# Optimization experiments

Hardware: AMD Instinct MI355X
Metric: run time of the kernel (lower is better)

The kernel has to match this reference:

```python
import jax, jax.numpy as jnp
import numpy as np

B, S, DIM_IN, DIM_K, DIM_V = 4, 2048, 512, 2048, 64


def setup_inputs() -> dict:
    key = jax.random.key(0)
    k1, k2, k3, k4 = jax.random.split(key, 4)
    x = jax.random.normal(k1, (B, S, DIM_IN), dtype=jnp.float32)
    # nn.Linear(dim_in, d, bias=False) -> stored transposed here so y = x @ W
    Wq = jax.random.normal(k2, (DIM_IN, DIM_K), dtype=jnp.float32) / np.sqrt(DIM_IN)
    Wk = jax.random.normal(k3, (DIM_IN, DIM_K), dtype=jnp.float32) / np.sqrt(DIM_IN)
    Wv = jax.random.normal(k4, (DIM_IN, DIM_V), dtype=jnp.float32) / np.sqrt(DIM_IN)
    return {"x": x, "Wq": Wq, "Wk": Wk, "Wv": Wv}


def reference(x, Wq, Wk, Wv):
    dim_k = Wq.shape[-1]
    q = x @ Wq            # [B, S, dim_k]
    k = x @ Wk            # [B, S, dim_k]
    v = x @ Wv            # [B, S, dim_v]
    scores = jnp.einsum("bqd,bkd->bqk", q, k)  # [B, S, S]
    # causal mask: disallow attending to strictly-future positions
    seq = scores.shape[-1]
    mask = jnp.triu(jnp.ones((seq, seq), dtype=bool), k=1)
    scores = jnp.where(mask[None, :, :], -jnp.inf, scores)
    attn = jax.nn.softmax(scores / np.sqrt(dim_k).astype(np.float32), axis=-1)
    return attn @ v       # [B, S, dim_v]
```

## Files before the change

kernel.cpp:

```cpp
#include <hip/hip_runtime.h>
#include <hip/hip_bf16.h>
#include <math.h>

using bf16 = __hip_bfloat16;
typedef __bf16 bf16x8 __attribute__((ext_vector_type(8)));
typedef float floatx4 __attribute__((ext_vector_type(4)));

constexpr int BB = 4, SS = 2048, DIN = 512, DKK = 2048, DVV = 64;
constexpr int ROWS = BB * SS;
constexpr int LDY = 640;

constexpr size_t XB_OFF  = 0;
constexpr size_t WQB_OFF = XB_OFF  + 8388608;
constexpr size_t WKB_OFF = WQB_OFF + 2097152;
constexpr size_t WT2_OFF = WKB_OFF + 2097152;
constexpr size_t MTP_OFF = WT2_OFF + 655360;
constexpr size_t YV_OFF  = MTP_OFF + 8388608;
constexpr size_t VT_OFF  = YV_OFF  + 10485760;
constexpr size_t PRT_OFF = VT_OFF  + 1048576;
constexpr size_t STA_OFF = PRT_OFF + 16777216;

__device__ __forceinline__ void async_copy16(const bf16* g, const unsigned short* l) {
    __builtin_amdgcn_global_load_lds((const __attribute__((address_space(1))) void*)g,
                                     (__attribute__((address_space(3))) void*)l, 16, 0, 0);
}

__global__ __launch_bounds__(256) void prep(const float* __restrict__ x,
                                            const float* __restrict__ Wq,
                                            const float* __restrict__ Wk,
                                            const float* __restrict__ Wv,
                                            bf16* __restrict__ xb,
                                            bf16* __restrict__ wqb,
                                            bf16* __restrict__ wkb,
                                            bf16* __restrict__ wt2) {
    __shared__ float tile[32][33];
    const int bid = blockIdx.x;
    const int tid = threadIdx.x;

    if (bid < 4096) {
        int i = bid * 256 + tid;
        float4 v = reinterpret_cast<const float4*>(x)[i];
        union { bf16 h[4]; ushort4 u; } cv;
        cv.h[0] = __float2bfloat16(v.x);
        cv.h[1] = __float2bfloat16(v.y);
        cv.h[2] = __float2bfloat16(v.z);
        cv.h[3] = __float2bfloat16(v.w);
        reinterpret_cast<ushort4*>(xb)[i] = cv.u;
    } else if (bid < 6144) {
        int i = (bid - 4096) * 256 + tid;
        const float* src = (i < 262144) ? Wq : Wk;
        bf16* dst = (i < 262144) ? wqb : wkb;
        int j = (i < 262144) ? i : i - 262144;
        float4 v = reinterpret_cast<const float4*>(src)[j];
        union { bf16 h[4]; ushort4 u; } cv;
        cv.h[0] = __float2bfloat16(v.x);
        cv.h[1] = __float2bfloat16(v.y);
        cv.h[2] = __float2bfloat16(v.z);
        cv.h[3] = __float2bfloat16(v.w);
        reinterpret_cast<ushort4*>(dst)[j] = cv.u;
    } else {
        int idx = bid - 6144;
        int n0 = (idx & 1) * 32;
        int k0 = (idx >> 1) * 32;
        int nn = tid & 31, kk8 = tid >> 5;
        #pragma unroll
        for (int p = 0; p < 4; ++p) {
            int k = p * 8 + kk8;
            tile[k][nn] = Wv[(long long)(k0 + k) * 64 + n0 + nn];
        }
        __syncthreads();
        int kk = tid & 31, nn8 = tid >> 5;
        #pragma unroll
        for (int p = 0; p < 4; ++p) {
            int n = p * 8 + nn8;
            wt2[(long long)(512 + n0 + n) * 512 + k0 + kk] = __float2bfloat16(tile[kk][n]);
        }
    }
}

__global__ __launch_bounds__(256) void gemm_mt(const bf16* __restrict__ A,
                                               const bf16* __restrict__ Bt,
                                               float* __restrict__ Cp) {
    __shared__ __align__(16) unsigned short As[128 * 64];
    __shared__ __align__(16) unsigned short Bs[128 * 64];

    const int tid = threadIdx.x;
    const int lane = tid & 63, wave = tid >> 6;

    const int wg = (blockIdx.x & 7) * 16 + (blockIdx.x >> 3);
    const int z = wg >> 4;
    const int tile = wg & 15;
    const long long m0 = (long long)(tile >> 2) * 128;
    const long long n0 = (long long)(tile & 3) * 128;
    const int koff = z * 256;

    const int rIn = lane >> 3;
    const int cSwz = ((lane & 7) ^ rIn) * 8;
    const int wm0 = (wave >> 1) * 64, wn0 = (wave & 1) * 64;
    const int l15 = lane & 15, quad = lane >> 4;
    const int sw7 = l15 & 7;

    floatx4 acc[4][4] = {};

    for (int k0 = koff; k0 < koff + 256; k0 += 64) {
        #pragma unroll
        for (int t0 = 0; t0 < 8; ++t0) {
            int t = t0 * 4 + wave;
            if (t < 16)
                async_copy16(A + (m0 + t * 8 + rIn) * 2048LL + k0 + cSwz, &As[t * 512]);
            else
                async_copy16(Bt + (n0 + (t - 16) * 8 + rIn) * 2048LL + k0 + cSwz, &Bs[(t - 16) * 512]);
        }
        __syncthreads();
        #pragma unroll
        for (int sk = 0; sk < 2; ++sk) {
            const int rchunk = (((sk << 2) | quad) ^ sw7) * 8;
            bf16x8 af[4], bfr[4];
            #pragma unroll
            for (int mi = 0; mi < 4; ++mi)
                af[mi] = *reinterpret_cast<const bf16x8*>(&As[(wm0 + mi * 16 + l15) * 64 + rchunk]);
            #pragma unroll
            for (int ni = 0; ni < 4; ++ni)
                bfr[ni] = *reinterpret_cast<const bf16x8*>(&Bs[(wn0 + ni * 16 + l15) * 64 + rchunk]);
            #pragma unroll
            for (int mi = 0; mi < 4; ++mi)
                #pragma unroll
                for (int ni = 0; ni < 4; ++ni)
                    acc[mi][ni] = __builtin_amdgcn_mfma_f32_16x16x32_bf16(af[mi], bfr[ni],
                                                                          acc[mi][ni], 0, 0, 0);
        }
        __syncthreads();
    }

    float* C = Cp + (long long)z * 262144;
    #pragma unroll
    for (int mi = 0; mi < 4; ++mi) {
        long long row0 = m0 + wm0 + mi * 16 + quad * 4;
        #pragma unroll
        for (int ni = 0; ni < 4; ++ni) {
            long long col = n0 + wn0 + ni * 16 + l15;
            #pragma unroll
            for (int r = 0; r < 4; ++r)
                C[(row0 + r) * 512 + col] = acc[mi][ni][r];
        }
    }
}

__global__ __launch_bounds__(256) void reduce_mt(const float4* __restrict__ part,
                                                 bf16* __restrict__ wt2) {
    int i = blockIdx.x * 256 + threadIdx.x;
    float4 s = {0.f, 0.f, 0.f, 0.f};
    #pragma unroll
    for (int t = 0; t < 8; ++t) {
        float4 a = part[(long long)t * 65536 + i];
        s.x += a.x; s.y += a.y; s.z += a.z; s.w += a.w;
    }
    union { bf16 h[4]; ushort4 u; } cv;
    cv.h[0] = __float2bfloat16(s.x);
    cv.h[1] = __float2bfloat16(s.y);
    cv.h[2] = __float2bfloat16(s.z);
    cv.h[3] = __float2bfloat16(s.w);
    reinterpret_cast<ushort4*>(wt2)[i] = cv.u;
}

__global__ __launch_bounds__(256) void gemm_proj(const bf16* __restrict__ A,
                                                 const bf16* __restrict__ Bt,
                                                 bf16* __restrict__ C,
                                                 bf16* __restrict__ vt) {
    __shared__ __align__(16) unsigned short As[128 * 64];
    __shared__ __align__(16) unsigned short Bs[128 * 64];

    const int tid = threadIdx.x;
    const int lane = tid & 63, wave = tid >> 6;

    const int wg = (blockIdx.x & 7) * 40 + (blockIdx.x >> 3);
    const long long m0 = (long long)(wg / 5) * 128;
    const long long n0 = (long long)(wg % 5) * 128;

    const int rIn = lane >> 3;
    const int cSwz = ((lane & 7) ^ rIn) * 8;
    const int wm0 = (wave >> 1) * 64, wn0 = (wave & 1) * 64;
    const int l15 = lane & 15, quad = lane >> 4;
    const int sw7 = l15 & 7;

    floatx4 acc[4][4] = {};

    for (int k0 = 0; k0 < DIN; k0 += 64) {
        #pragma unroll
        for (int t0 = 0; t0 < 8; ++t0) {
            int t = t0 * 4 + wave;
            if (t < 16)
                async_copy16(A + (m0 + t * 8 + rIn) * (long long)DIN + k0 + cSwz, &As[t * 512]);
            else
                async_copy16(Bt + (n0 + (t - 16) * 8 + rIn) * (long long)DIN + k0 + cSwz, &Bs[(t - 16) * 512]);
        }
        __syncthreads();
        #pragma unroll
        for (int sk = 0; sk < 2; ++sk) {
            const int rchunk = (((sk << 2) | quad) ^ sw7) * 8;
            bf16x8 af[4], bfr[4];
            #pragma unroll
            for (int mi = 0; mi < 4; ++mi)
                af[mi] = *reinterpret_cast<const bf16x8*>(&As[(wm0 + mi * 16 + l15) * 64 + rchunk]);
            #pragma unroll
            for (int ni = 0; ni < 4; ++ni)
                bfr[ni] = *reinterpret_cast<const bf16x8*>(&Bs[(wn0 + ni * 16 + l15) * 64 + rchunk]);
            #pragma unroll
            for (int mi = 0; mi < 4; ++mi)
                #pragma unroll
                for (int ni = 0; ni < 4; ++ni)
                    acc[mi][ni] = __builtin_amdgcn_mfma_f32_16x16x32_bf16(af[mi], bfr[ni],
                                                                          acc[mi][ni], 0, 0, 0);
        }
        __syncthreads();
    }

    if (n0 < 512) {
        #pragma unroll
        for (int mi = 0; mi < 4; ++mi) {
            long long row0 = m0 + wm0 + mi * 16 + quad * 4;
            #pragma unroll
            for (int ni = 0; ni < 4; ++ni) {
                long long col = n0 + wn0 + ni * 16 + l15;
                #pragma unroll
                for (int r = 0; r < 4; ++r)
                    C[(row0 + r) * (long long)LDY + col] = __float2bfloat16(acc[mi][ni][r]);
            }
        }
    } else if (!(wave & 1)) {
        const int b = (int)(m0 >> 11);
        const int sbase = ((int)m0 & 2047) + wm0;
        #pragma unroll
        for (int mi = 0; mi < 4; ++mi) {
            int s0 = sbase + mi * 16 + quad * 4;
            #pragma unroll
            for (int ni = 0; ni < 4; ++ni) {
                int j = ni * 16 + l15;
                union { bf16 h[4]; ushort4 u; } cv;
                #pragma unroll
                for (int r = 0; r < 4; ++r)
                    cv.h[r] = __float2bfloat16(acc[mi][ni][r]);
                *reinterpret_cast<ushort4*>(vt + ((long long)(b * DVV + j)) * SS + s0) = cv.u;
            }
        }
    }
}

__global__ __launch_bounds__(512) void attn_fused(const bf16* __restrict__ yv,
                                                  const bf16* __restrict__ xb,
                                                  const bf16* __restrict__ vt,
                                                  bf16* __restrict__ part,
                                                  float* __restrict__ stats) {
    constexpr int BK = 64;
    constexpr float SCALE = 0.022097086912079608f;

    __shared__ __align__(16) char smem[65536];
    unsigned short* As = (unsigned short*)smem;
    unsigned short* Bs = (unsigned short*)(smem + 32768);
    unsigned short* Ps = (unsigned short*)smem;
    unsigned short* Vs = (unsigned short*)(smem + 34816);
    float* smax = (float*)(smem + 52224);
    float* ssum = (float*)(smem + 53248);

    const int wg = (blockIdx.x & 7) * 17 + (blockIdx.x >> 3);
    int by = (int)((sqrtf(8.f * (float)wg + 1.f) - 1.f) * 0.5f);
    while ((by + 1) * (by + 2) / 2 <= wg) ++by;
    while (by * (by + 1) / 2 > wg) --by;
    const int bx = wg - by * (by + 1) / 2;
    const int b = blockIdx.z;

    const bf16* A  = yv + (long long)b * SS * LDY;
    const bf16* Bt = xb + (long long)b * SS * 512;

    const int tid = threadIdx.x;
    const int lane = tid & 63, wave = tid >> 6;
    const long long m0 = (long long)by * 128;
    const long long n0 = (long long)bx * 128;

    const int rIn = lane >> 3;
    const int cSwz = ((lane & 7) ^ rIn) * 8;
    const int wm0 = (wave >> 1) * 32, wn0 = (wave & 1) * 64;
    const int l15 = lane & 15, quad = lane >> 4;
    const int sw7 = l15 & 7;

    floatx4 acc[2][4] = {};

    uint4 vreg[2];
    #pragma unroll
    for (int p = 0; p < 2; ++p) {
        int j = (tid >> 4) + p * 32;
        int ch = tid & 15;
        vreg[p] = *reinterpret_cast<const uint4*>(
            vt + ((long long)b * DVV + j) * SS + n0 + ch * 8);
    }

    auto issue = [&](int buf, int k0) {
        #pragma unroll
        for (int t0 = 0; t0 < 4; ++t0) {
            int t = t0 * 8 + wave;
            if (t < 16)
                async_copy16(A + (m0 + t * 8 + rIn) * (long long)LDY + k0 + cSwz,
                             &As[buf * 8192 + t * 512]);
            else
                async_copy16(Bt + (n0 + (t - 16) * 8 + rIn) * 512LL + k0 + cSwz,
                             &Bs[buf * 8192 + (t - 16) * 512]);
        }
    };

    issue(0, 0);
    __syncthreads();
    for (int it = 0; it < DIN / BK; ++it) {
        const int cur = it & 1;
        if (it + 1 < DIN / BK) issue(cur ^ 1, (it + 1) * BK);
        #pragma unroll
        for (int sk = 0; sk < 2; ++sk) {
            const int rchunk = ((sk << 2) | quad) ^ sw7;
            bf16x8 af[2], bfr[4];
            #pragma unroll
            for (int mi = 0; mi < 2; ++mi)
                af[mi] = *reinterpret_cast<const bf16x8*>(
                    &As[cur * 8192 + (wm0 + mi * 16 + l15) * BK + rchunk * 8]);
            #pragma unroll
            for (int ni = 0; ni < 4; ++ni)
                bfr[ni] = *reinterpret_cast<const bf16x8*>(
                    &Bs[cur * 8192 + (wn0 + ni * 16 + l15) * BK + rchunk * 8]);
            #pragma unroll
            for (int mi = 0; mi < 2; ++mi)
                #pragma unroll
                for (int ni = 0; ni < 4; ++ni)
                    acc[mi][ni] = __builtin_amdgcn_mfma_f32_16x16x32_bf16(af[mi], bfr[ni],
                                                                          acc[mi][ni], 0, 0, 0);
        }
        __syncthreads();
    }

    #pragma unroll
    for (int mi = 0; mi < 2; ++mi)
        #pragma unroll
        for (int ni = 0; ni < 4; ++ni)
            #pragma unroll
            for (int r = 0; r < 4; ++r) {
                float v = acc[mi][ni][r] * SCALE;
                if (bx == by) {
                    int row = wm0 + mi * 16 + quad * 4 + r;
                    int col = wn0 + ni * 16 + l15;
                    if (col > row) v = -INFINITY;
                }
                acc[mi][ni][r] = v;
            }

    float rmax[2][4];
    #pragma unroll
    for (int mi = 0; mi < 2; ++mi)
        #pragma unroll
        for (int r = 0; r < 4; ++r) {
            float m = fmaxf(fmaxf(acc[mi][0][r], acc[mi][1][r]),
                            fmaxf(acc[mi][2][r], acc[mi][3][r]));
            #pragma unroll
            for (int msk = 8; msk >= 1; msk >>= 1) m = fmaxf(m, __shfl_xor(m, msk));
            rmax[mi][r] = m;
            if (l15 == 0) smax[(wm0 + mi * 16 + quad * 4 + r) * 2 + (wave & 1)] = m;
        }
    __syncthreads();
    #pragma unroll
    for (int mi = 0; mi < 2; ++mi)
        #pragma unroll
        for (int r = 0; r < 4; ++r) {
            int row = wm0 + mi * 16 + quad * 4 + r;
            rmax[mi][r] = fmaxf(smax[row * 2], smax[row * 2 + 1]);
        }

    #pragma unroll
    for (int mi = 0; mi < 2; ++mi)
        #pragma unroll
        for (int r = 0; r < 4; ++r) {
            float s = 0.f;
            #pragma unroll
            for (int ni = 0; ni < 4; ++ni) {
                float p = __expf(acc[mi][ni][r] - rmax[mi][r]);
                acc[mi][ni][r] = p;
                s += p;
            }
            #pragma unroll
            for (int msk = 8; msk >= 1; msk >>= 1) s += __shfl_xor(s, msk);
            if (l15 == 0) ssum[(wm0 + mi * 16 + quad * 4 + r) * 2 + (wave & 1)] = s;
        }
    #pragma unroll
    for (int mi = 0; mi < 2; ++mi) {
        int row = wm0 + mi * 16 + quad * 4;
        #pragma unroll
        for (int ni = 0; ni < 4; ++ni) {
            int col = wn0 + ni * 16 + l15;
            #pragma unroll
            for (int r = 0; r < 4; ++r)
                Ps[(row + r) * 136 + col] = (unsigned short)__bfloat16_as_ushort(__float2bfloat16(acc[mi][ni][r]));
        }
    }

    #pragma unroll
    for (int p = 0; p < 2; ++p) {
        int j = (tid >> 4) + p * 32;
        int ch = tid & 15;
        *reinterpret_cast<uint4*>(&Vs[j * 136 + ((ch ^ (j & 7)) * 8)]) = vreg[p];
    }
    __syncthreads();

    if (tid < 128) {
        float m = fmaxf(smax[tid * 2], smax[tid * 2 + 1]);
        float l = ssum[tid * 2] + ssum[tid * 2 + 1];
        long long o = (((long long)b * 16 + bx) * SS + m0 + tid) * 2;
        stats[o] = m;
        stats[o + 1] = l;
    }

    const int wmv = wave * 16;
    floatx4 accO[4] = {};
    #pragma unroll
    for (int sk = 0; sk < 4; ++sk) {
        bf16x8 af = *reinterpret_cast<const bf16x8*>(
            &Ps[(wmv + l15) * 136 + sk * 32 + quad * 8]);
        #pragma unroll
        for (int ni = 0; ni < 4; ++ni) {
            bf16x8 bfv = *reinterpret_cast<const bf16x8*>(
                &Vs[(ni * 16 + l15) * 136 + ((((sk << 2) | quad)) ^ sw7) * 8]);
            accO[ni] = __builtin_amdgcn_mfma_f32_16x16x32_bf16(af, bfv, accO[ni], 0, 0, 0);
        }
    }
    #pragma unroll
    for (int ni = 0; ni < 4; ++ni)
        #pragma unroll
        for (int r = 0; r < 4; ++r)
            part[(((long long)b * 16 + bx) * SS + m0 + wmv + quad * 4 + r) * 64 + ni * 16 + l15]
                = __float2bfloat16(accO[ni][r]);
}

__global__ __launch_bounds__(256) void combine(const bf16* __restrict__ part,
                                               const float* __restrict__ stats,
                                               float* __restrict__ out) {
    int tid = blockIdx.x * 256 + threadIdx.x;
    int row = tid >> 3;
    int col8 = (tid & 7) * 8;
    int b = row >> 11, s = row & (SS - 1);
    int nt = (s >> 7) + 1;

    float m[16], l[16], M = -INFINITY;
    #pragma unroll
    for (int t = 0; t < 16; ++t)
        if (t < nt) {
            long long o = (((long long)b * 16 + t) * SS + s) * 2;
            m[t] = stats[o];
            l[t] = stats[o + 1];
            M = fmaxf(M, m[t]);
        }
    float O[8] = {};
    float L = 0.f;
    #pragma unroll
    for (int t = 0; t < 16; ++t)
        if (t < nt) {
            float wgt = __expf(m[t] - M);
            L += wgt * l[t];
            union { uint4 q; unsigned short u[8]; } ld;
            ld.q = *reinterpret_cast<const uint4*>(
                part + (((long long)b * 16 + t) * SS + s) * 64 + col8);
            #pragma unroll
            for (int j = 0; j < 8; ++j)
                O[j] += wgt * __uint_as_float((unsigned)ld.u[j] << 16);
        }
    float rinv = 1.0f / L;
    float4 o0 = {O[0] * rinv, O[1] * rinv, O[2] * rinv, O[3] * rinv};
    float4 o1 = {O[4] * rinv, O[5] * rinv, O[6] * rinv, O[7] * rinv};
    float4* dst = reinterpret_cast<float4*>(out + (long long)row * 64 + col8);
    dst[0] = o0;
    dst[1] = o1;
}

extern "C" void kernel_launch(void* const* d_in, const int* in_sizes, int n_in,
                              void* d_out, int out_size, void* d_ws, size_t ws_size,
                              hipStream_t stream) {
    const float* x  = (const float*)d_in[0];
    const float* Wq = (const float*)d_in[1];
    const float* Wk = (const float*)d_in[2];
    const float* Wv = (const float*)d_in[3];
    float* out = (float*)d_out;

    char* w = (char*)d_ws;
    bf16* xb   = (bf16*)(w + XB_OFF);
    bf16* wqb  = (bf16*)(w + WQB_OFF);
    bf16* wkb  = (bf16*)(w + WKB_OFF);
    bf16* wt2  = (bf16*)(w + WT2_OFF);
    float* mtp = (float*)(w + MTP_OFF);
    bf16* yv   = (bf16*)(w + YV_OFF);
    bf16* vt   = (bf16*)(w + VT_OFF);
    bf16* part = (bf16*)(w + PRT_OFF);
    float* stats = (float*)(w + STA_OFF);

    prep<<<6176, 256, 0, stream>>>(x, Wq, Wk, Wv, xb, wqb, wkb, wt2);

    gemm_mt<<<128, 256, 0, stream>>>(wkb, wqb, mtp);
    reduce_mt<<<65536 / 256, 256, 0, stream>>>((const float4*)mtp, wt2);

    gemm_proj<<<320, 256, 0, stream>>>(xb, wt2, yv, vt);

    attn_fused<<<dim3(136, 1, BB), 512, 0, stream>>>(yv, xb, vt, part, stats);

    combine<<<ROWS * 8 / 256, 256, 0, stream>>>(part, stats, out);
}
```

Before: 144.2 us.

## Single-buffer QK tiles and split P staging to cut LDS for occupancy

Drops the double-buffered A/B tiles in the QK^T main loop to a single buffer, issuing each load right before its barrier. The P tile is staged in two halves, first from the even waves and then from the odd waves, with an extra barrier between them. Together these shrink shared memory from 64KB to about 37KB so more workgroups can be resident per CU. The cost is that loads no longer overlap compute within a workgroup, so latency hiding now depends on other resident workgroups. s_setprio hints are also added around the MFMA sections.

```diff
diff --git a/kernel.cpp b/kernel.cpp
--- a/kernel.cpp
+++ b/kernel.cpp
@@ -254,13 +254,13 @@
     constexpr int BK = 64;
     constexpr float SCALE = 0.022097086912079608f;
 
-    __shared__ __align__(16) char smem[65536];
+    __shared__ __align__(16) char smem[37888];
     unsigned short* As = (unsigned short*)smem;
-    unsigned short* Bs = (unsigned short*)(smem + 32768);
+    unsigned short* Bs = (unsigned short*)(smem + 16384);
     unsigned short* Ps = (unsigned short*)smem;
-    unsigned short* Vs = (unsigned short*)(smem + 34816);
-    float* smax = (float*)(smem + 52224);
-    float* ssum = (float*)(smem + 53248);
+    unsigned short* Vs = (unsigned short*)(smem + 18432);
+    float* smax = (float*)(smem + 35840);
+    float* ssum = (float*)(smem + 36864);
 
     const int wg = (blockIdx.x & 7) * 17 + (blockIdx.x >> 3);
     int by = (int)((sqrtf(8.f * (float)wg + 1.f) - 1.f) * 0.5f);
@@ -294,24 +294,23 @@
             vt + ((long long)b * DVV + j) * SS + n0 + ch * 8);
     }
 
-    auto issue = [&](int buf, int k0) {
+    auto issue = [&](int k0) {
         #pragma unroll
         for (int t0 = 0; t0 < 4; ++t0) {
             int t = t0 * 8 + wave;
             if (t < 16)
                 async_copy16(A + (m0 + t * 8 + rIn) * (long long)LDY + k0 + cSwz,
-                             &As[buf * 8192 + t * 512]);
+                             &As[t * 512]);
             else
                 async_copy16(Bt + (n0 + (t - 16) * 8 + rIn) * 512LL + k0 + cSwz,
-                             &Bs[buf * 8192 + (t - 16) * 512]);
+                             &Bs[(t - 16) * 512]);
         }
     };
 
-    issue(0, 0);
-    __syncthreads();
     for (int it = 0; it < DIN / BK; ++it) {
-        const int cur = it & 1;
-        if (it + 1 < DIN / BK) issue(cur ^ 1, (it + 1) * BK);
+        issue(it * BK);
+        __syncthreads();
+        __builtin_amdgcn_s_setprio(1);
         #pragma unroll
         for (int sk = 0; sk < 2; ++sk) {
             const int rchunk = ((sk << 2) | quad) ^ sw7;
@@ -319,11 +318,11 @@
             #pragma unroll
             for (int mi = 0; mi < 2; ++mi)
                 af[mi] = *reinterpret_cast<const bf16x8*>(
-                    &As[cur * 8192 + (wm0 + mi * 16 + l15) * BK + rchunk * 8]);
+                    &As[(wm0 + mi * 16 + l15) * BK + rchunk * 8]);
             #pragma unroll
             for (int ni = 0; ni < 4; ++ni)
                 bfr[ni] = *reinterpret_cast<const bf16x8*>(
-                    &Bs[cur * 8192 + (wn0 + ni * 16 + l15) * BK + rchunk * 8]);
+                    &Bs[(wn0 + ni * 16 + l15) * BK + rchunk * 8]);
             #pragma unroll
             for (int mi = 0; mi < 2; ++mi)
                 #pragma unroll
@@ -331,6 +330,7 @@
                     acc[mi][ni] = __builtin_amdgcn_mfma_f32_16x16x32_bf16(af[mi], bfr[ni],
                                                                           acc[mi][ni], 0, 0, 0);
         }
+        __builtin_amdgcn_s_setprio(0);
         __syncthreads();
     }
 
@@ -385,18 +385,21 @@
             for (int msk = 8; msk >= 1; msk >>= 1) s += __shfl_xor(s, msk);
             if (l15 == 0) ssum[(wm0 + mi * 16 + quad * 4 + r) * 2 + (wave & 1)] = s;
         }
-    #pragma unroll
-    for (int mi = 0; mi < 2; ++mi) {
-        int row = wm0 + mi * 16 + quad * 4;
-        #pragma unroll
-        for (int ni = 0; ni < 4; ++ni) {
-            int col = wn0 + ni * 16 + l15;
-            #pragma unroll
-            for (int r = 0; r < 4; ++r)
-                Ps[(row + r) * 136 + col] = (unsigned short)__bfloat16_as_ushort(__float2bfloat16(acc[mi][ni][r]));
-        }
-    }
-
+
+    if ((wave & 1) == 0) {
+        #pragma unroll
+        for (int mi = 0; mi < 2; ++mi) {
+            int row = wm0 + mi * 16 + quad * 4;
+            #pragma unroll
+            for (int ni = 0; ni < 4; ++ni) {
+                int col = ni * 16 + l15;
+                #pragma unroll
+                for (int r = 0; r < 4; ++r)
+                    Ps[(row + r) * 72 + col] =
+                        (unsigned short)__bfloat16_as_ushort(__float2bfloat16(acc[mi][ni][r]));
+            }
+        }
+    }
     #pragma unroll
     for (int p = 0; p < 2; ++p) {
         int j = (tid >> 4) + p * 32;
@@ -415,17 +418,52 @@
 
     const int wmv = wave * 16;
     floatx4 accO[4] = {};
-    #pragma unroll
-    for (int sk = 0; sk < 4; ++sk) {
+    __builtin_amdgcn_s_setprio(1);
+    #pragma unroll
+    for (int sk = 0; sk < 2; ++sk) {
         bf16x8 af = *reinterpret_cast<const bf16x8*>(
-            &Ps[(wmv + l15) * 136 + sk * 32 + quad * 8]);
+            &Ps[(wmv + l15) * 72 + sk * 32 + quad * 8]);
         #pragma unroll
         for (int ni = 0; ni < 4; ++ni) {
             bf16x8 bfv = *reinterpret_cast<const bf16x8*>(
-                &Vs[(ni * 16 + l15) * 136 + ((((sk << 2) | quad)) ^ sw7) * 8]);
+                &Vs[(ni * 16 + l15) * 136 + (((sk << 2) | quad) ^ sw7) * 8]);
             accO[ni] = __builtin_amdgcn_mfma_f32_16x16x32_bf16(af, bfv, accO[ni], 0, 0, 0);
         }
     }
+    __builtin_amdgcn_s_setprio(0);
+    __syncthreads();
+
+    if ((wave & 1) == 1) {
+        #pragma unroll
+        for (int mi = 0; mi < 2; ++mi) {
+            int row = wm0 + mi * 16 + quad * 4;
+            #pragma unroll
+            for (int ni = 0; ni < 4; ++ni) {
+                int col = ni * 16 + l15;
+                #pragma unroll
+                for (int r = 0; r < 4; ++r)
+                    Ps[(row + r) * 72 + col] =
+                        (unsigned short)__bfloat16_as_ushort(__float2bfloat16(acc[mi][ni][r]));
+            }
+        }
+    }
+    __syncthreads();
+
+    __builtin_amdgcn_s_setprio(1);
+    #pragma unroll
+    for (int sk = 0; sk < 2; ++sk) {
+        const int kc = 2 + sk;
+        bf16x8 af = *reinterpret_cast<const bf16x8*>(
+            &Ps[(wmv + l15) * 72 + sk * 32 + quad * 8]);
+        #pragma unroll
+        for (int ni = 0; ni < 4; ++ni) {
+            bf16x8 bfv = *reinterpret_cast<const bf16x8*>(
+                &Vs[(ni * 16 + l15) * 136 + (((kc << 2) | quad) ^ sw7) * 8]);
+            accO[ni] = __builtin_amdgcn_mfma_f32_16x16x32_bf16(af, bfv, accO[ni], 0, 0, 0);
+        }
+    }
+    __builtin_amdgcn_s_setprio(0);
+
     #pragma unroll
     for (int ni = 0; ni < 4; ++ni)
         #pragma unroll
```

Measured after the change: 141.3 us. -2.0%, faster.
